# Optimization experiments

Measured on AMD Instinct MI355X. Metric: run time of the kernel, lower is better.

## Reference

```python
import math
import jax, jax.numpy as jnp
import numpy as np

B, S, OBS, ACT, D, H, F, L = 4, 512, 64, 16, 1024, 16, 4096, 4
T = 2 * S - 1  # 1023


def setup_inputs() -> dict:
    key = jax.random.key(0)
    ks = iter(jax.random.split(key, 48))
    def nrm(shape, scale=0.02):
        return (jax.random.normal(next(ks), shape, dtype=jnp.float32) * scale)
    z = lambda *s: jnp.zeros(s, jnp.float32)
    o = lambda *s: jnp.ones(s, jnp.float32)
    inp = {
        'observations': jax.random.normal(next(ks), (B, S, OBS), jnp.float32),
        'actions': jax.random.normal(next(ks), (B, S - 1, ACT), jnp.float32),
        # input_fc: obs_size -> D -> D -> D
        'in_w1': nrm((OBS, D)), 'in_b1': z(D), 'in_w2': nrm((D, D)), 'in_b2': z(D), 'in_w3': nrm((D, D)), 'in_b3': z(D),
        # action_fc: action_size -> D -> D -> D
        'act_w1': nrm((ACT, D)), 'act_b1': z(D), 'act_w2': nrm((D, D)), 'act_b2': z(D), 'act_w3': nrm((D, D)), 'act_b3': z(D),
        # output_fc: D -> D -> D -> action_size
        'out_w1': nrm((D, D)), 'out_b1': z(D), 'out_w2': nrm((D, D)), 'out_b2': z(D), 'out_w3': nrm((D, ACT)), 'out_b3': z(ACT),
        # decoder self-attn (stacked over L layers)
        'sa_w_in': nrm((L, D, 3 * D)), 'sa_b_in': z(L, 3 * D), 'sa_w_out': nrm((L, D, D)), 'sa_b_out': z(L, D),
        # decoder cross-attn
        'ca_w_in': nrm((L, D, 3 * D)), 'ca_b_in': z(L, 3 * D), 'ca_w_out': nrm((L, D, D)), 'ca_b_out': z(L, D),
        # decoder FFN
        'ff_w1': nrm((L, D, F)), 'ff_b1': z(L, F), 'ff_w2': nrm((L, F, D)), 'ff_b2': z(L, D),
        # layer norms
        'ln1_g': o(L, D), 'ln1_b': z(L, D), 'ln2_g': o(L, D), 'ln2_b': z(L, D), 'ln3_g': o(L, D), 'ln3_b': z(L, D),
        'lnf_g': o(D), 'lnf_b': z(D),
    }
    return inp


def _mlp(x, w1, b1, w2, b2, w3, b3):
    x = jax.nn.relu(x @ w1 + b1)
    x = jax.nn.relu(x @ w2 + b2)
    return x @ w3 + b3


def _ln(x, g, b, eps=1e-5):
    mu = x.mean(-1, keepdims=True)
    var = ((x - mu) ** 2).mean(-1, keepdims=True)
    return (x - mu) * jax.lax.rsqrt(var + eps) * g + b


def _mha(q_in, kv_in, w_in, b_in, w_out, b_out, mask):
    Bq, Tq, Dm = q_in.shape
    Tk = kv_in.shape[1]
    dh = Dm // H
    q = q_in @ w_in[:, :Dm] + b_in[:Dm]
    k = kv_in @ w_in[:, Dm:2 * Dm] + b_in[Dm:2 * Dm]
    v = kv_in @ w_in[:, 2 * Dm:] + b_in[2 * Dm:]
    q = q.reshape(Bq, Tq, H, dh).transpose(0, 2, 1, 3)
    k = k.reshape(Bq, Tk, H, dh).transpose(0, 2, 1, 3)
    v = v.reshape(Bq, Tk, H, dh).transpose(0, 2, 1, 3)
    s = jnp.einsum('bhqd,bhkd->bhqk', q, k) / math.sqrt(dh)
    if mask is not None:
        s = s + mask
    a = jax.nn.softmax(s, axis=-1)
    out = jnp.einsum('bhqk,bhkd->bhqd', a, v).transpose(0, 2, 1, 3).reshape(Bq, Tq, Dm)
    return out @ w_out + b_out


def reference(observations, actions,
              in_w1, in_b1, in_w2, in_b2, in_w3, in_b3,
              act_w1, act_b1, act_w2, act_b2, act_w3, act_b3,
              out_w1, out_b1, out_w2, out_b2, out_w3, out_b3,
              sa_w_in, sa_b_in, sa_w_out, sa_b_out,
              ca_w_in, ca_b_in, ca_w_out, ca_b_out,
              ff_w1, ff_b1, ff_w2, ff_b2,
              ln1_g, ln1_b, ln2_g, ln2_b, ln3_g, ln3_b, lnf_g, lnf_b):
    obs_tok = _mlp(observations, in_w1, in_b1, in_w2, in_b2, in_w3, in_b3)   # [B,S,D]
    act_tok = _mlp(actions, act_w1, act_b1, act_w2, act_b2, act_w3, act_b3)  # [B,S-1,D]
    # fused interleave [obs1, act1, obs2, ..., obsS] (replaces the python loops)
    tgt = jnp.zeros((B, T, D), obs_tok.dtype).at[:, 0::2].set(obs_tok).at[:, 1::2].set(act_tok)
    # PositionalEncoding is applied on a batch-first tensor in the original code,
    # so pe[:x.size(0)] indexes by BATCH and broadcasts over the sequence dim (bug-faithful).
    pos = jnp.arange(B, dtype=jnp.float32)[:, None]
    div = jnp.exp(jnp.arange(0, D, 2, dtype=jnp.float32) * (-math.log(10000.0) / D))
    pe = jnp.stack([jnp.sin(pos * div), jnp.cos(pos * div)], axis=-1).reshape(B, D)
    x = tgt + pe[:, None, :]
    mask = jnp.triu(jnp.full((T, T), -jnp.inf, dtype=jnp.float32), k=1)
    mem = jnp.zeros((B, 1, D), x.dtype)  # inp_tok (zero memory token)
    for l in range(L):  # post-norm nn.TransformerDecoderLayer, dropout=0
        x = _ln(x + _mha(x, x, sa_w_in[l], sa_b_in[l], sa_w_out[l], sa_b_out[l], mask), ln1_g[l], ln1_b[l])
        x = _ln(x + _mha(x, mem, ca_w_in[l], ca_b_in[l], ca_w_out[l], ca_b_out[l], None), ln2_g[l], ln2_b[l])
        ff = jax.nn.relu(x @ ff_w1[l] + ff_b1[l]) @ ff_w2[l] + ff_b2[l]
        x = _ln(x + ff, ln3_g[l], ln3_b[l])
    x = _ln(x, lnf_g, lnf_b)  # nn.Transformer final decoder norm
    return _mlp(x, out_w1, out_b1, out_w2, out_b2, out_w3, out_b3)  # [B,T,action_size]
```

## Files before the change

### kernel.cpp

```cpp
#include <hip/hip_runtime.h>
#include <hip/hip_bf16.h>
#include <cstdint>
#include <cstddef>

#define B_  4
#define S_  512
#define T_  1023
#define D_  1024
#define H_  16
#define DH_ 64
#define F_  4096
#define L_  4

typedef float f32x4 __attribute__((ext_vector_type(4)));
typedef __bf16 bf16x8 __attribute__((ext_vector_type(8)));

__device__ inline unsigned pack_bf2(float a, float b) {
    union { __hip_bfloat16 h; unsigned short u; } ua, ub;
    ua.h = __float2bfloat16(a); ub.h = __float2bfloat16(b);
    return (unsigned)ua.u | ((unsigned)ub.u << 16);
}

__global__ __launch_bounds__(256) void gemm_bf16(
    const __hip_bfloat16* __restrict__ A, const __hip_bfloat16* __restrict__ Wt,
    const float* __restrict__ bias,
    float* __restrict__ Cf, __hip_bfloat16* __restrict__ Cb,
    int M, int K, int N, int relu, int ksplit)
{
    __shared__ __align__(16) __hip_bfloat16 AsmB[3][128 * 32];
    __shared__ __align__(16) __hip_bfloat16 BsmB[3][64 * 32];
    const int tid  = threadIdx.x;
    const int lane = tid & 63;
    const int w    = tid >> 6;
    const int wr   = w >> 1, wc = w & 1;
    const int l15  = lane & 15, l4 = lane >> 4;

    const int gx = gridDim.x;
    int bid = blockIdx.y * gx + blockIdx.x;
    {
        const int nwg = gx * gridDim.y;
        const int q = nwg >> 3, r = nwg & 7;
        const int xcd = bid & 7, idx = bid >> 3;
        bid = (xcd < r ? xcd * (q + 1) : r * (q + 1) + (xcd - r) * q) + idx;
    }
    const int row0 = (bid / gx) * 128;
    const int col0 = (bid % gx) * 64;
    const int z = blockIdx.z;
    const int kslice = K / ksplit;
    const int kbase = z * kslice;

    f32x4 acc[4][2] = {};

    auto stage = [&](__hip_bfloat16* As, __hip_bfloat16* Bs, int kt) {
        auto* ldsA = (__attribute__((address_space(3))) char*)As;
        auto* ldsB = (__attribute__((address_space(3))) char*)Bs;
        #pragma unroll
        for (int half = 0; half < 2; ++half) {
            const int ch = half * 256 + tid;
            const int r  = ch >> 2;
            const int c  = (ch & 3) * 8;
            int gr = row0 + r; gr = (gr < M) ? gr : (M - 1);
            const __hip_bfloat16* srcA = A + (size_t)gr * K + kt + c;
            __builtin_amdgcn_global_load_lds(
                (const __attribute__((address_space(1))) unsigned*)srcA,
                (__attribute__((address_space(3))) unsigned*)(ldsA + (size_t)ch * 16),
                16, 0, 0);
        }
        {
            const int r = tid >> 2;
            const int c = (tid & 3) * 8;
            int gc = col0 + r; gc = (gc < N) ? gc : (N - 1);
            const __hip_bfloat16* srcB = Wt + (size_t)gc * K + kt + c;
            __builtin_amdgcn_global_load_lds(
                (const __attribute__((address_space(1))) unsigned*)srcB,
                (__attribute__((address_space(3))) unsigned*)(ldsB + (size_t)tid * 16),
                16, 0, 0);
        }
    };
    auto compute = [&](const __hip_bfloat16* As, const __hip_bfloat16* Bs) {
        const __hip_bfloat16* ab = As + (size_t)(wr * 64 + l15) * 32 + l4 * 8;
        const __hip_bfloat16* bb = Bs + (size_t)(wc * 32 + l15) * 32 + l4 * 8;
        bf16x8 af[4], bf[2];
        #pragma unroll
        for (int mi = 0; mi < 4; ++mi) af[mi] = *(const bf16x8*)(ab + mi * 16 * 32);
        #pragma unroll
        for (int nj = 0; nj < 2; ++nj) bf[nj] = *(const bf16x8*)(bb + nj * 16 * 32);
        #pragma unroll
        for (int mi = 0; mi < 4; ++mi)
            #pragma unroll
            for (int nj = 0; nj < 2; ++nj)
                acc[mi][nj] = __builtin_amdgcn_mfma_f32_16x16x32_bf16(
                    af[mi], bf[nj], acc[mi][nj], 0, 0, 0);
    };

    const int nk = kslice >> 5;
    __hip_bfloat16 *A0 = AsmB[0], *A1 = AsmB[1], *A2 = AsmB[2];
    __hip_bfloat16 *B0 = BsmB[0], *B1 = BsmB[1], *B2 = BsmB[2];
    stage(A0, B0, kbase);
    if (nk > 1) stage(A1, B1, kbase + 32);
    for (int t = 0; t < nk; ++t) {
        if (t + 1 < nk) {
            asm volatile("s_waitcnt vmcnt(3)" ::: "memory");
        } else {
            asm volatile("s_waitcnt vmcnt(0)" ::: "memory");
        }
        __builtin_amdgcn_s_barrier();
        if (t + 2 < nk) stage(A2, B2, kbase + (t + 2) * 32);
        compute(A0, B0);
        __hip_bfloat16* ta = A0; A0 = A1; A1 = A2; A2 = ta;
        __hip_bfloat16* tb = B0; B0 = B1; B1 = B2; B2 = tb;
    }

    if (ksplit > 1) {
        float* dst = Cf + (size_t)z * M * N;
        #pragma unroll
        for (int nj = 0; nj < 2; ++nj) {
            const int c = col0 + wc * 32 + nj * 16 + l15;
            if (c >= N) continue;
            #pragma unroll
            for (int mi = 0; mi < 4; ++mi)
                #pragma unroll
                for (int i = 0; i < 4; ++i) {
                    const int r = row0 + wr * 64 + mi * 16 + l4 * 4 + i;
                    if (r < M) dst[(size_t)r * N + c] = acc[mi][nj][i];
                }
        }
    } else {
        #pragma unroll
        for (int nj = 0; nj < 2; ++nj) {
            const int c = col0 + wc * 32 + nj * 16 + l15;
            if (c >= N) continue;
            const float bv = bias[c];
            #pragma unroll
            for (int mi = 0; mi < 4; ++mi)
                #pragma unroll
                for (int i = 0; i < 4; ++i) {
                    const int r = row0 + wr * 64 + mi * 16 + l4 * 4 + i;
                    if (r >= M) continue;
                    float v = acc[mi][nj][i] + bv;
                    if (relu) v = fmaxf(v, 0.f);
                    if (Cf) Cf[(size_t)r * N + c] = v;
                    if (Cb) Cb[(size_t)r * N + c] = __float2bfloat16(v);
                }
        }
    }
}

__global__ __launch_bounds__(256) void reduce_split(
    const float* __restrict__ part, int SK, size_t pstride,
    const float* __restrict__ bias, int N, int total4, int relu,
    float* __restrict__ outf, __hip_bfloat16* __restrict__ outb)
{
    const int idx4 = blockIdx.x * 256 + threadIdx.x;
    if (idx4 >= total4) return;
    const size_t base = (size_t)idx4 * 4;
    const int c = (int)(base & (size_t)(N - 1));
    float4 v = *(const float4*)(part + base);
    for (int s = 1; s < SK; ++s) {
        const float4 p = *(const float4*)(part + (size_t)s * pstride + base);
        v.x += p.x; v.y += p.y; v.z += p.z; v.w += p.w;
    }
    const float4 bv = *(const float4*)(bias + c);
    v.x += bv.x; v.y += bv.y; v.z += bv.z; v.w += bv.w;
    if (relu) {
        v.x = fmaxf(v.x, 0.f); v.y = fmaxf(v.y, 0.f);
        v.z = fmaxf(v.z, 0.f); v.w = fmaxf(v.w, 0.f);
    }
    if (outf) *(float4*)(outf + base) = v;
    if (outb) {
        __hip_bfloat16* o = outb + base;
        o[0] = __float2bfloat16(v.x); o[1] = __float2bfloat16(v.y);
        o[2] = __float2bfloat16(v.z); o[3] = __float2bfloat16(v.w);
    }
}

__global__ __launch_bounds__(256) void transpose_w(
    const float* __restrict__ W, __hip_bfloat16* __restrict__ Wt,
    int K, int N, int Kpad)
{
    __shared__ float t[32][33];
    W  += (size_t)blockIdx.z * K * N;
    Wt += (size_t)blockIdx.z * N * Kpad;
    const int n0 = blockIdx.x * 32, k0 = blockIdx.y * 32;
    const int tx = threadIdx.x & 31, ty = threadIdx.x >> 5;
    #pragma unroll
    for (int i = 0; i < 4; ++i) {
        int r = ty + i * 8;
        int k = k0 + r, n = n0 + tx;
        t[r][tx] = (k < K && n < N) ? W[(size_t)k * N + n] : 0.f;
    }
    __syncthreads();
    #pragma unroll
    for (int i = 0; i < 4; ++i) {
        int r = ty + i * 8;
        int n = n0 + r, k = k0 + tx;
        if (n < N && k < Kpad) Wt[(size_t)n * Kpad + k] = __float2bfloat16(t[tx][r]);
    }
}

__global__ __launch_bounds__(256) void convert_pad(
    const float* __restrict__ in, __hip_bfloat16* __restrict__ out,
    int M, int Kin, int Kout)
{
    int idx = blockIdx.x * 256 + threadIdx.x;
    if (idx >= M * Kout) return;
    int r = idx / Kout, c = idx - r * Kout;
    out[idx] = __float2bfloat16(c < Kin ? in[(size_t)r * Kin + c] : 0.f);
}

__global__ __launch_bounds__(256) void v_transpose(
    const __hip_bfloat16* __restrict__ qkvb, __hip_bfloat16* __restrict__ vt)
{
    __shared__ __hip_bfloat16 tile[32][33];
    const int b  = blockIdx.z;
    const int c0 = blockIdx.x * 32;
    const int t0 = blockIdx.y * 32;
    const int tx = threadIdx.x & 31, ty = threadIdx.x >> 5;
    const __hip_bfloat16 z = __float2bfloat16(0.f);
    #pragma unroll
    for (int i = 0; i < 4; ++i) {
        const int tl = ty + i * 8;
        const int t = t0 + tl;
        tile[tl][tx] = (t < T_) ? qkvb[(size_t)(b * T_ + t) * 3072 + 2048 + c0 + tx] : z;
    }
    __syncthreads();
    #pragma unroll
    for (int i = 0; i < 4; ++i) {
        const int cl = ty + i * 8;
        const int t = t0 + tx;
        vt[((size_t)(b * 1024 + c0 + cl)) * 1024 + t] = (t < T_) ? tile[tx][cl] : z;
    }
}

__global__ __launch_bounds__(256) void attn_mfma(
    const __hip_bfloat16* __restrict__ qkvb,
    const __hip_bfloat16* __restrict__ vt,
    __hip_bfloat16* __restrict__ out)
{
    __shared__ __align__(16) __hip_bfloat16 Qs[2][128][32];
    __shared__ __align__(16) __hip_bfloat16 Ks[2][64][32];
    __shared__ __align__(16) __hip_bfloat16 Vs[2][64][32];
    __shared__ __align__(16) __hip_bfloat16 Ps[4][2][32][32];
    __shared__ float Lw[4][2][16];

    const int bh = blockIdx.x;
    const int b = bh >> 4, h = bh & 15;
    const int q0 = blockIdx.y * 128;
    const int tid = threadIdx.x;
    const int w = tid >> 6, lane = tid & 63;
    const int l15 = lane & 15, l4 = lane >> 4;
    const size_t ldq = 3 * D_;

    {
        #pragma unroll
        for (int c = 0; c < 2; ++c)
            #pragma unroll
            for (int it = 0; it < 2; ++it) {
                const int ch = it * 256 + tid;
                const int r = ch >> 2, cp = ch & 3;
                int qr = q0 + r; qr = (qr < T_) ? qr : (T_ - 1);
                const __hip_bfloat16* src = qkvb + (size_t)(b * T_ + qr) * ldq + h * 64 + c * 32 + cp * 8;
                __builtin_amdgcn_global_load_lds(
                    (const __attribute__((address_space(1))) unsigned*)src,
                    (__attribute__((address_space(3))) unsigned*)((__attribute__((address_space(3))) char*)&Qs[c][0][0] + ch * 16),
                    16, 0, 0);
            }
    }
    __syncthreads();
    bf16x8 qreg[2][2];
    #pragma unroll
    for (int qf = 0; qf < 2; ++qf)
        #pragma unroll
        for (int c = 0; c < 2; ++c)
            qreg[qf][c] = *(const bf16x8*)&Qs[c][w * 32 + qf * 16 + l15][l4 * 8];

    f32x4 of[2][4] = {};
    float lp[2] = {0.f, 0.f};
    const int qmaxw = q0 + w * 32 + 31;
    const int kend = (q0 + 128 < T_) ? (q0 + 128) : T_;

    for (int k0 = 0; k0 < kend; k0 += 64) {
        __syncthreads();
        {
            const int r = tid >> 2, cp = tid & 3;
            #pragma unroll
            for (int c = 0; c < 2; ++c) {
                int kr = k0 + r; kr = (kr < T_) ? kr : (T_ - 1);
                const __hip_bfloat16* srcK = qkvb + (size_t)(b * T_ + kr) * ldq + D_ + h * 64 + c * 32 + cp * 8;
                __builtin_amdgcn_global_load_lds(
                    (const __attribute__((address_space(1))) unsigned*)srcK,
                    (__attribute__((address_space(3))) unsigned*)((__attribute__((address_space(3))) char*)&Ks[c][0][0] + tid * 16),
                    16, 0, 0);
                const __hip_bfloat16* srcV = vt + ((size_t)(b * 1024 + h * 64 + r)) * 1024 + k0 + c * 32 + cp * 8;
                __builtin_amdgcn_global_load_lds(
                    (const __attribute__((address_space(1))) unsigned*)srcV,
                    (__attribute__((address_space(3))) unsigned*)((__attribute__((address_space(3))) char*)&Vs[c][0][0] + tid * 16),
                    16, 0, 0);
            }
        }
        __syncthreads();

        if (k0 <= qmaxw) {
            f32x4 sf[4][2] = {};
            #pragma unroll
            for (int c = 0; c < 2; ++c) {
                bf16x8 kf[4];
                #pragma unroll
                for (int kfr = 0; kfr < 4; ++kfr)
                    kf[kfr] = *(const bf16x8*)&Ks[c][kfr * 16 + l15][l4 * 8];
                #pragma unroll
                for (int kfr = 0; kfr < 4; ++kfr)
                    #pragma unroll
                    for (int qf = 0; qf < 2; ++qf)
                        sf[kfr][qf] = __builtin_amdgcn_mfma_f32_16x16x32_bf16(
                            kf[kfr], qreg[qf][c], sf[kfr][qf], 0, 0, 0);
            }
            const bool needmask = (k0 + 63) > (q0 + w * 32);
            #pragma unroll
            for (int kfr = 0; kfr < 4; ++kfr) {
                #pragma unroll
                for (int qf = 0; qf < 2; ++qf) {
                    const int qg = q0 + w * 32 + qf * 16 + l15;
                    float p[4];
                    #pragma unroll
                    for (int i = 0; i < 4; ++i) {
                        const int kg = k0 + kfr * 16 + l4 * 4 + i;
                        float pv = __expf(sf[kfr][qf][i] * 0.125f);
                        if (needmask && kg > qg) pv = 0.f;
                        p[i] = pv;
                        lp[qf] += pv;
                    }
                    unsigned* dst = (unsigned*)&Ps[w][kfr >> 1][qf * 16 + l15][(kfr & 1) * 16 + l4 * 4];
                    dst[0] = pack_bf2(p[0], p[1]);
                    dst[1] = pack_bf2(p[2], p[3]);
                }
            }
            #pragma unroll
            for (int kc = 0; kc < 2; ++kc) {
                bf16x8 pa[2], vb[4];
                #pragma unroll
                for (int qf = 0; qf < 2; ++qf)
                    pa[qf] = *(const bf16x8*)&Ps[w][kc][qf * 16 + l15][l4 * 8];
                #pragma unroll
                for (int df = 0; df < 4; ++df)
                    vb[df] = *(const bf16x8*)&Vs[kc][df * 16 + l15][l4 * 8];
                #pragma unroll
                for (int qf = 0; qf < 2; ++qf)
                    #pragma unroll
                    for (int df = 0; df < 4; ++df)
                        of[qf][df] = __builtin_amdgcn_mfma_f32_16x16x32_bf16(
                            pa[qf], vb[df], of[qf][df], 0, 0, 0);
            }
        }
    }

    #pragma unroll
    for (int qf = 0; qf < 2; ++qf) {
        float v = lp[qf];
        v += __shfl_xor(v, 16);
        v += __shfl_xor(v, 32);
        if (l4 == 0) Lw[w][qf][l15] = v;
    }
    __syncthreads();
    #pragma unroll
    for (int qf = 0; qf < 2; ++qf) {
        float inv[4];
        #pragma unroll
        for (int i = 0; i < 4; ++i) inv[i] = 1.f / Lw[w][qf][l4 * 4 + i];
        #pragma unroll
        for (int df = 0; df < 4; ++df) {
            #pragma unroll
            for (int i = 0; i < 4; ++i) {
                const int qg = q0 + w * 32 + qf * 16 + l4 * 4 + i;
                if (qg < T_)
                    out[(size_t)(b * T_ + qg) * D_ + h * 64 + df * 16 + l15] =
                        __float2bfloat16(of[qf][df][i] * inv[i]);
            }
        }
    }
}

__device__ inline void block_ln_stats(float4 v, float& mu, float& inv,
                                      float* ws, float* ws2, float* mu_s, float* inv_s)
{
    const int tid = threadIdx.x;
    float s  = v.x + v.y + v.z + v.w;
    float s2 = v.x * v.x + v.y * v.y + v.z * v.z + v.w * v.w;
    #pragma unroll
    for (int off = 32; off; off >>= 1) {
        s  += __shfl_down(s, off);
        s2 += __shfl_down(s2, off);
    }
    const int wid = tid >> 6;
    if ((tid & 63) == 0) { ws[wid] = s; ws2[wid] = s2; }
    __syncthreads();
    if (tid == 0) {
        float S  = ws[0] + ws[1] + ws[2] + ws[3];
        float S2 = ws2[0] + ws2[1] + ws2[2] + ws2[3];
        float m = S * (1.f / (float)D_);
        float var = S2 * (1.f / (float)D_) - m * m;
        *mu_s = m;
        *inv_s = rsqrtf(var + 1e-5f);
    }
    __syncthreads();
    mu = *mu_s; inv = *inv_s;
}

__global__ __launch_bounds__(256) void add_ln_kernel(
    float* __restrict__ x, const float* __restrict__ p, int SK, size_t pstride,
    const float* __restrict__ pbias,
    const float* __restrict__ g, const float* __restrict__ beta,
    __hip_bfloat16* __restrict__ xb)
{
    const int row = blockIdx.x;
    const int tid = threadIdx.x;
    __shared__ float ws[4], ws2[4], mu_s, inv_s;
    float4* xr = reinterpret_cast<float4*>(x + (size_t)row * D_);
    float4 v = xr[tid];
    if (p) {
        for (int s = 0; s < SK; ++s) {
            const float4 wv = reinterpret_cast<const float4*>(
                p + (size_t)s * pstride + (size_t)row * D_)[tid];
            v.x += wv.x; v.y += wv.y; v.z += wv.z; v.w += wv.w;
        }
        if (pbias) {
            const float4 bv = reinterpret_cast<const float4*>(pbias)[tid];
            v.x += bv.x; v.y += bv.y; v.z += bv.z; v.w += bv.w;
        }
    }
    float mu, inv;
    block_ln_stats(v, mu, inv, ws, ws2, &mu_s, &inv_s);
    const float4 gg = reinterpret_cast<const float4*>(g)[tid];
    const float4 bb = reinterpret_cast<const float4*>(beta)[tid];
    float4 o;
    o.x = (v.x - mu) * inv * gg.x + bb.x;
    o.y = (v.y - mu) * inv * gg.y + bb.y;
    o.z = (v.z - mu) * inv * gg.z + bb.z;
    o.w = (v.w - mu) * inv * gg.w + bb.w;
    xr[tid] = o;
    if (xb) {
        __hip_bfloat16* xo = xb + (size_t)row * D_ + tid * 4;
        xo[0] = __float2bfloat16(o.x);
        xo[1] = __float2bfloat16(o.y);
        xo[2] = __float2bfloat16(o.z);
        xo[3] = __float2bfloat16(o.w);
    }
}

__global__ __launch_bounds__(256) void add_ln2_kernel(
    float* __restrict__ x, const float* __restrict__ p, int SK, size_t pstride,
    const float* __restrict__ pbias, const float* __restrict__ cav,
    const float* __restrict__ g1, const float* __restrict__ b1,
    const float* __restrict__ g2, const float* __restrict__ b2,
    __hip_bfloat16* __restrict__ xb)
{
    const int row = blockIdx.x;
    const int tid = threadIdx.x;
    __shared__ float ws[4], ws2[4], mu_s, inv_s;
    float4* xr = reinterpret_cast<float4*>(x + (size_t)row * D_);
    float4 v = xr[tid];
    for (int s = 0; s < SK; ++s) {
        const float4 wv = reinterpret_cast<const float4*>(
            p + (size_t)s * pstride + (size_t)row * D_)[tid];
        v.x += wv.x; v.y += wv.y; v.z += wv.z; v.w += wv.w;
    }
    if (pbias) {
        const float4 bv = reinterpret_cast<const float4*>(pbias)[tid];
        v.x += bv.x; v.y += bv.y; v.z += bv.z; v.w += bv.w;
    }
    float mu, inv;
    block_ln_stats(v, mu, inv, ws, ws2, &mu_s, &inv_s);
    const float4 g1v = reinterpret_cast<const float4*>(g1)[tid];
    const float4 b1v = reinterpret_cast<const float4*>(b1)[tid];
    const float4 cv  = reinterpret_cast<const float4*>(cav)[tid];
    float4 u;
    u.x = (v.x - mu) * inv * g1v.x + b1v.x + cv.x;
    u.y = (v.y - mu) * inv * g1v.y + b1v.y + cv.y;
    u.z = (v.z - mu) * inv * g1v.z + b1v.z + cv.z;
    u.w = (v.w - mu) * inv * g1v.w + b1v.w + cv.w;
    __syncthreads();
    float mu2, inv2;
    block_ln_stats(u, mu2, inv2, ws, ws2, &mu_s, &inv_s);
    const float4 g2v = reinterpret_cast<const float4*>(g2)[tid];
    const float4 b2v = reinterpret_cast<const float4*>(b2)[tid];
    float4 o;
    o.x = (u.x - mu2) * inv2 * g2v.x + b2v.x;
    o.y = (u.y - mu2) * inv2 * g2v.y + b2v.y;
    o.z = (u.z - mu2) * inv2 * g2v.z + b2v.z;
    o.w = (u.w - mu2) * inv2 * g2v.w + b2v.w;
    xr[tid] = o;
    __hip_bfloat16* xo = xb + (size_t)row * D_ + tid * 4;
    xo[0] = __float2bfloat16(o.x);
    xo[1] = __float2bfloat16(o.y);
    xo[2] = __float2bfloat16(o.z);
    xo[3] = __float2bfloat16(o.w);
}

__global__ __launch_bounds__(256) void interleave_pe_kernel(
    const float* __restrict__ obs_tok, const float* __restrict__ act_tok,
    float* __restrict__ x, __hip_bfloat16* __restrict__ xb)
{
    const int row = blockIdx.x;
    const int b = row / T_;
    const int t = row - b * T_;
    const float* src = (t & 1)
        ? (act_tok + (size_t)(b * (S_ - 1) + (t >> 1)) * D_)
        : (obs_tok + (size_t)(b * S_ + (t >> 1)) * D_);
    float* xr = x + (size_t)row * D_;
    __hip_bfloat16* xo = xb + (size_t)row * D_;
    #pragma unroll
    for (int k = 0; k < 4; ++k) {
        int d = threadIdx.x + k * 256;
        float ang = (float)b * expf(-(float)(d & ~1) * (9.210340371976184f / 1024.0f));
        float pe = (d & 1) ? cosf(ang) : sinf(ang);
        float v = src[d] + pe;
        xr[d] = v;
        xo[d] = __float2bfloat16(v);
    }
}

__global__ __launch_bounds__(256) void ca_part_kernel(
    const float* __restrict__ ca_b_in, const float* __restrict__ ca_w_out,
    float* __restrict__ part)
{
    const int idx = blockIdx.x * 256 + threadIdx.x;
    const int ks = blockIdx.y;
    const int l = idx >> 10, d = idx & 1023;
    const float* bv = ca_b_in + (size_t)l * 3 * D_ + 2 * D_ + ks * 64;
    const float* wp = ca_w_out + (size_t)l * D_ * D_ + (size_t)(ks * 64) * D_ + d;
    float s = 0.f;
    #pragma unroll 8
    for (int k = 0; k < 64; ++k) s = fmaf(bv[k], wp[(size_t)k * D_], s);
    part[(size_t)ks * (L_ * D_) + idx] = s;
}

__global__ __launch_bounds__(256) void ca_reduce_kernel(
    const float* __restrict__ part, const float* __restrict__ ca_b_out,
    float* __restrict__ out)
{
    const int idx = blockIdx.x * 256 + threadIdx.x;
    float s = ca_b_out[idx];
    #pragma unroll
    for (int ks = 0; ks < 16; ++ks) s += part[(size_t)ks * (L_ * D_) + idx];
    out[idx] = s;
}

extern "C" void kernel_launch(void* const* d_in, const int* in_sizes, int n_in,
                              void* d_out, int out_size, void* d_ws, size_t ws_size,
                              hipStream_t stream)
{
    const float* obs     = (const float*)d_in[0];
    const float* act     = (const float*)d_in[1];
    const float* in_w1   = (const float*)d_in[2];
    const float* in_b1   = (const float*)d_in[3];
    const float* in_w2   = (const float*)d_in[4];
    const float* in_b2   = (const float*)d_in[5];
    const float* in_w3   = (const float*)d_in[6];
    const float* in_b3   = (const float*)d_in[7];
    const float* act_w1  = (const float*)d_in[8];
    const float* act_b1  = (const float*)d_in[9];
    const float* act_w2  = (const float*)d_in[10];
    const float* act_b2  = (const float*)d_in[11];
    const float* act_w3  = (const float*)d_in[12];
    const float* act_b3  = (const float*)d_in[13];
    const float* out_w1  = (const float*)d_in[14];
    const float* out_b1  = (const float*)d_in[15];
    const float* out_w2  = (const float*)d_in[16];
    const float* out_b2  = (const float*)d_in[17];
    const float* out_w3  = (const float*)d_in[18];
    const float* out_b3  = (const float*)d_in[19];
    const float* sa_w_in = (const float*)d_in[20];
    const float* sa_b_in = (const float*)d_in[21];
    const float* sa_w_out= (const float*)d_in[22];
    const float* sa_b_out= (const float*)d_in[23];
    const float* ca_b_in = (const float*)d_in[25];
    const float* ca_w_out= (const float*)d_in[26];
    const float* ca_b_out= (const float*)d_in[27];
    const float* ff_w1   = (const float*)d_in[28];
    const float* ff_b1   = (const float*)d_in[29];
    const float* ff_w2   = (const float*)d_in[30];
    const float* ff_b2   = (const float*)d_in[31];
    const float* ln1_g   = (const float*)d_in[32];
    const float* ln1_b   = (const float*)d_in[33];
    const float* ln2_g   = (const float*)d_in[34];
    const float* ln2_b   = (const float*)d_in[35];
    const float* ln3_g   = (const float*)d_in[36];
    const float* ln3_b   = (const float*)d_in[37];
    const float* lnf_g   = (const float*)d_in[38];
    const float* lnf_b   = (const float*)d_in[39];

    const int MT = B_ * T_;
    const int Mo = B_ * S_;
    const int Ma = B_ * (S_ - 1);

    char* base = (char*)d_ws;
    size_t used = 0;
    auto alloc = [&](size_t bytes) -> char* {
        char* r = base + used;
        used += (bytes + 255) & ~(size_t)255;
        return r;
    };
    typedef __hip_bfloat16 bf;
    bf* wi1  = (bf*)alloc((size_t)1024 * 64 * 2);
    bf* wi2  = (bf*)alloc((size_t)1024 * 1024 * 2);
    bf* wi3  = (bf*)alloc((size_t)1024 * 1024 * 2);
    bf* wa1  = (bf*)alloc((size_t)1024 * 32 * 2);
    bf* wa2  = (bf*)alloc((size_t)1024 * 1024 * 2);
    bf* wa3  = (bf*)alloc((size_t)1024 * 1024 * 2);
    bf* wo1  = (bf*)alloc((size_t)1024 * 1024 * 2);
    bf* wo2  = (bf*)alloc((size_t)1024 * 1024 * 2);
    bf* wo3  = (bf*)alloc((size_t)16 * 1024 * 2);
    bf* wsin = (bf*)alloc((size_t)L_ * 3072 * 1024 * 2);
    bf* wsout= (bf*)alloc((size_t)L_ * 1024 * 1024 * 2);
    bf* wf1  = (bf*)alloc((size_t)L_ * 4096 * 1024 * 2);
    bf* wf2  = (bf*)alloc((size_t)L_ * 1024 * 4096 * 2);
    bf* obs_bf = (bf*)alloc((size_t)Mo * 64 * 2);
    bf* act_bf = (bf*)alloc((size_t)Ma * 32 * 2);
    bf* x_bf   = (bf*)alloc((size_t)MT * D_ * 2);
    bf* attnb  = (bf*)alloc((size_t)MT * D_ * 2);
    bf* h1b    = (bf*)alloc((size_t)MT * D_ * 2);
    bf* h2b    = (bf*)alloc((size_t)MT * D_ * 2);
    char* shared_rg = alloc((size_t)MT * F_ * 2);
    bf* qkvb = (bf*)shared_rg;
    bf* ffh  = (bf*)shared_rg;
    bf* vt   = (bf*)alloc((size_t)B_ * 1024 * 1024 * 2);
    float* x       = (float*)alloc((size_t)MT * D_ * 4);
    float* y       = (float*)alloc((size_t)MT * D_ * 4);
    float* obs_tok = (float*)alloc((size_t)Mo * D_ * 4);
    float* act_tok = (float*)alloc((size_t)Ma * D_ * 4);
    float* ca      = (float*)alloc((size_t)L_ * D_ * 4);
    float* ca_part = (float*)alloc((size_t)16 * L_ * D_ * 4);
    if (used > ws_size) return;
    float* part_loop = y;
    float* part_pre  = (float*)shared_rg;
    float* part_post = (float*)shared_rg;

    auto tw = [&](const float* W, bf* Wt, int K, int N, int Kpad, int batch) {
        dim3 g((N + 31) / 32, (Kpad + 31) / 32, batch);
        transpose_w<<<g, 256, 0, stream>>>(W, Wt, K, N, Kpad);
    };
    auto gemm = [&](const bf* A, const bf* Wt, const float* bias,
                    float* Cf, bf* Cb, int M, int K, int N, int relu, int sk) {
        dim3 g((N + 63) / 64, (M + 127) / 128, sk);
        gemm_bf16<<<g, 256, 0, stream>>>(A, Wt, bias, Cf, Cb, M, K, N, relu, sk);
    };
    auto gemm_red = [&](const bf* A, const bf* Wt, const float* bias,
                        float* Cf, bf* Cb, int M, int K, int N, int relu, int sk,
                        float* part) {
        if (sk <= 1) { gemm(A, Wt, bias, Cf, Cb, M, K, N, relu, 1); return; }
        gemm(A, Wt, nullptr, part, nullptr, M, K, N, 0, sk);
        const size_t MN = (size_t)M * N;
        const int total4 = (int)(MN / 4);
        reduce_split<<<(total4 + 255) / 256, 256, 0, stream>>>(
            part, sk, MN, bias, N, total4, relu, Cf, Cb);
    };

    tw(in_w1,  wi1, 64,   1024, 64,   1);
    tw(in_w2,  wi2, 1024, 1024, 1024, 1);
    tw(in_w3,  wi3, 1024, 1024, 1024, 1);
    tw(act_w1, wa1, 16,   1024, 32,   1);
    tw(act_w2, wa2, 1024, 1024, 1024, 1);
    tw(act_w3, wa3, 1024, 1024, 1024, 1);
    tw(out_w1, wo1, 1024, 1024, 1024, 1);
    tw(out_w2, wo2, 1024, 1024, 1024, 1);
    tw(out_w3, wo3, 1024, 16,   1024, 1);
    tw(sa_w_in,  wsin,  1024, 3072, 1024, L_);
    tw(sa_w_out, wsout, 1024, 1024, 1024, L_);
    tw(ff_w1,    wf1,   1024, 4096, 1024, L_);
    tw(ff_w2,    wf2,   4096, 1024, 4096, L_);

    convert_pad<<<(Mo * 64 + 255) / 256, 256, 0, stream>>>(obs, obs_bf, Mo, 64, 64);
    convert_pad<<<(Ma * 32 + 255) / 256, 256, 0, stream>>>(act, act_bf, Ma, 16, 32);
    ca_part_kernel<<<dim3((L_ * D_) / 256, 16), 256, 0, stream>>>(ca_b_in, ca_w_out, ca_part);
    ca_reduce_kernel<<<(L_ * D_) / 256, 256, 0, stream>>>(ca_part, ca_b_out, ca);

    gemm(obs_bf, wi1, in_b1, nullptr, h1b, Mo, 64, D_, 1, 1);
    gemm_red(h1b, wi2, in_b2, nullptr, h2b, Mo, D_, D_, 1, 4, part_pre);
    gemm_red(h2b, wi3, in_b3, obs_tok, nullptr, Mo, D_, D_, 0, 4, part_pre);
    gemm(act_bf, wa1, act_b1, nullptr, h1b, Ma, 32, D_, 1, 1);
    gemm_red(h1b, wa2, act_b2, nullptr, h2b, Ma, D_, D_, 1, 4, part_pre);
    gemm_red(h2b, wa3, act_b3, act_tok, nullptr, Ma, D_, D_, 0, 4, part_pre);

    interleave_pe_kernel<<<MT, 256, 0, stream>>>(obs_tok, act_tok, x, x_bf);

    for (int l = 0; l < L_; ++l) {
        gemm(x_bf, wsin + (size_t)l * 3072 * 1024, sa_b_in + (size_t)l * 3 * D_,
             nullptr, qkvb, MT, D_, 3 * D_, 0, 1);
        v_transpose<<<dim3(32, 32, B_), 256, 0, stream>>>(qkvb, vt);
        attn_mfma<<<dim3(B_ * H_, 8), 256, 0, stream>>>(qkvb, vt, attnb);
        gemm(attnb, wsout + (size_t)l * 1024 * 1024, nullptr,
             part_loop, nullptr, MT, D_, D_, 0, 2);
        add_ln2_kernel<<<MT, 256, 0, stream>>>(x, part_loop, 2, (size_t)MT * D_,
             sa_b_out + (size_t)l * D_, ca + (size_t)l * D_,
             ln1_g + (size_t)l * D_, ln1_b + (size_t)l * D_,
             ln2_g + (size_t)l * D_, ln2_b + (size_t)l * D_, x_bf);
        gemm(x_bf, wf1 + (size_t)l * 4096 * 1024, ff_b1 + (size_t)l * F_,
             nullptr, ffh, MT, D_, F_, 1, 1);
        gemm(ffh, wf2 + (size_t)l * 1024 * 4096, nullptr,
             part_loop, nullptr, MT, F_, D_, 0, 2);
        add_ln_kernel<<<MT, 256, 0, stream>>>(x, part_loop, 2, (size_t)MT * D_,
             ff_b2 + (size_t)l * D_,
             ln3_g + (size_t)l * D_, ln3_b + (size_t)l * D_, x_bf);
    }

    add_ln_kernel<<<MT, 256, 0, stream>>>(x, nullptr, 0, 0, nullptr, lnf_g, lnf_b, x_bf);
    gemm_red(x_bf, wo1, out_b1, nullptr, h1b, MT, D_, D_, 1, 2, part_post);
    gemm_red(h1b,  wo2, out_b2, nullptr, h2b, MT, D_, D_, 1, 2, part_post);
    gemm_red(h2b,  wo3, out_b3, (float*)d_out, nullptr, MT, D_, 16, 0, 8, part_post);
}
```

Baseline: 1.428 ms.

## Batch obs/action MLP GEMMs into paired launches and batch square weight transposes

Merges the observation and action input MLP GEMMs into single paired launches, with the z grid dimension selecting branch and split-K slice, plus a paired reduce kernel. It also folds ten 1024x1024 weight transposes into one launch. The goal is fewer kernel launches and better GPU fill for the small M=2048 GEMMs. Split-K drops from 4 to 2, so each block does more serial K work. The paired buffers assume h1b, h2b and part_pre are large enough to hold both halves.

```diff
diff --git a/kernel.cpp b/kernel.cpp
--- a/kernel.cpp
+++ b/kernel.cpp
@@ -146,6 +146,176 @@
     }
 }
 
+__global__ __launch_bounds__(256) void gemm_pair(
+    const __hip_bfloat16* __restrict__ A0p, const __hip_bfloat16* __restrict__ A1p,
+    const __hip_bfloat16* __restrict__ W0p, const __hip_bfloat16* __restrict__ W1p,
+    const float* __restrict__ b0p, const float* __restrict__ b1p,
+    __hip_bfloat16* __restrict__ Cb0, __hip_bfloat16* __restrict__ Cb1,
+    float* __restrict__ part,
+    int M0, int M1, int K0, int K1, int N, int relu, int sk)
+{
+    __shared__ __align__(16) __hip_bfloat16 AsmB[3][128 * 32];
+    __shared__ __align__(16) __hip_bfloat16 BsmB[3][64 * 32];
+    const int tid  = threadIdx.x;
+    const int lane = tid & 63;
+    const int w    = tid >> 6;
+    const int wr   = w >> 1, wc = w & 1;
+    const int l15  = lane & 15, l4 = lane >> 4;
+
+    const int gx = gridDim.x;
+    int bid = blockIdx.y * gx + blockIdx.x;
+    {
+        const int nwg = gx * gridDim.y;
+        const int q = nwg >> 3, r = nwg & 7;
+        const int xcd = bid & 7, idx = bid >> 3;
+        bid = (xcd < r ? xcd * (q + 1) : r * (q + 1) + (xcd - r) * q) + idx;
+    }
+    const int row0 = (bid / gx) * 128;
+    const int col0 = (bid % gx) * 64;
+
+    const int z = blockIdx.z;
+    const int pair  = z / sk;
+    const int slice = z - pair * sk;
+    const __hip_bfloat16* A  = pair ? A1p : A0p;
+    const __hip_bfloat16* Wt = pair ? W1p : W0p;
+    const float* bias        = pair ? b1p : b0p;
+    const int M = pair ? M1 : M0;
+    const int K = pair ? K1 : K0;
+    const int kslice = K / sk;
+    const int kbase = slice * kslice;
+
+    f32x4 acc[4][2] = {};
+
+    auto stage = [&](__hip_bfloat16* As, __hip_bfloat16* Bs, int kt) {
+        auto* ldsA = (__attribute__((address_space(3))) char*)As;
+        auto* ldsB = (__attribute__((address_space(3))) char*)Bs;
+        #pragma unroll
+        for (int half = 0; half < 2; ++half) {
+            const int ch = half * 256 + tid;
+            const int r  = ch >> 2;
+            const int c  = (ch & 3) * 8;
+            int gr = row0 + r; gr = (gr < M) ? gr : (M - 1);
+            const __hip_bfloat16* srcA = A + (size_t)gr * K + kt + c;
+            __builtin_amdgcn_global_load_lds(
+                (const __attribute__((address_space(1))) unsigned*)srcA,
+                (__attribute__((address_space(3))) unsigned*)(ldsA + (size_t)ch * 16),
+                16, 0, 0);
+        }
+        {
+            const int r = tid >> 2;
+            const int c = (tid & 3) * 8;
+            int gc = col0 + r; gc = (gc < N) ? gc : (N - 1);
+            const __hip_bfloat16* srcB = Wt + (size_t)gc * K + kt + c;
+            __builtin_amdgcn_global_load_lds(
+                (const __attribute__((address_space(1))) unsigned*)srcB,
+                (__attribute__((address_space(3))) unsigned*)(ldsB + (size_t)tid * 16),
+                16, 0, 0);
+        }
+    };
+    auto compute = [&](const __hip_bfloat16* As, const __hip_bfloat16* Bs) {
+        const __hip_bfloat16* ab = As + (size_t)(wr * 64 + l15) * 32 + l4 * 8;
+        const __hip_bfloat16* bb = Bs + (size_t)(wc * 32 + l15) * 32 + l4 * 8;
+        bf16x8 af[4], bf[2];
+        #pragma unroll
+        for (int mi = 0; mi < 4; ++mi) af[mi] = *(const bf16x8*)(ab + mi * 16 * 32);
+        #pragma unroll
+        for (int nj = 0; nj < 2; ++nj) bf[nj] = *(const bf16x8*)(bb + nj * 16 * 32);
+        #pragma unroll
+        for (int mi = 0; mi < 4; ++mi)
+            #pragma unroll
+            for (int nj = 0; nj < 2; ++nj)
+                acc[mi][nj] = __builtin_amdgcn_mfma_f32_16x16x32_bf16(
+                    af[mi], bf[nj], acc[mi][nj], 0, 0, 0);
+    };
+
+    const int nk = kslice >> 5;
+    __hip_bfloat16 *A0 = AsmB[0], *A1 = AsmB[1], *A2 = AsmB[2];
+    __hip_bfloat16 *B0 = BsmB[0], *B1 = BsmB[1], *B2 = BsmB[2];
+    stage(A0, B0, kbase);
+    if (nk > 1) stage(A1, B1, kbase + 32);
+    for (int t = 0; t < nk; ++t) {
+        if (t + 1 < nk) {
+            asm volatile("s_waitcnt vmcnt(3)" ::: "memory");
+        } else {
+            asm volatile("s_waitcnt vmcnt(0)" ::: "memory");
+        }
+        __builtin_amdgcn_s_barrier();
+        if (t + 2 < nk) stage(A2, B2, kbase + (t + 2) * 32);
+        compute(A0, B0);
+        __hip_bfloat16* ta = A0; A0 = A1; A1 = A2; A2 = ta;
+        __hip_bfloat16* tb = B0; B0 = B1; B1 = B2; B2 = tb;
+    }
+
+    if (sk > 1) {
+        const size_t pstride = (size_t)M0 * N;
+        float* dst = part + (size_t)(pair * sk + slice) * pstride;
+        #pragma unroll
+        for (int nj = 0; nj < 2; ++nj) {
+            const int c = col0 + wc * 32 + nj * 16 + l15;
+            #pragma unroll
+            for (int mi = 0; mi < 4; ++mi)
+                #pragma unroll
+                for (int i = 0; i < 4; ++i) {
+                    const int r = row0 + wr * 64 + mi * 16 + l4 * 4 + i;
+                    if (r < M) dst[(size_t)r * N + c] = acc[mi][nj][i];
+                }
+        }
+    } else {
+        __hip_bfloat16* Cb = pair ? Cb1 : Cb0;
+        #pragma unroll
+        for (int nj = 0; nj < 2; ++nj) {
+            const int c = col0 + wc * 32 + nj * 16 + l15;
+            const float bv = bias[c];
+            #pragma unroll
+            for (int mi = 0; mi < 4; ++mi)
+                #pragma unroll
+                for (int i = 0; i < 4; ++i) {
+                    const int r = row0 + wr * 64 + mi * 16 + l4 * 4 + i;
+                    if (r >= M) continue;
+                    float v = acc[mi][nj][i] + bv;
+                    if (relu) v = fmaxf(v, 0.f);
+                    Cb[(size_t)r * N + c] = __float2bfloat16(v);
+                }
+        }
+    }
+}
+
+__global__ __launch_bounds__(256) void reduce_pair(
+    const float* __restrict__ part, size_t pstride, int sk,
+    const float* __restrict__ b0p, const float* __restrict__ b1p,
+    int M0, int M1, int N, int relu,
+    __hip_bfloat16* __restrict__ ob0, __hip_bfloat16* __restrict__ ob1,
+    float* __restrict__ of0, float* __restrict__ of1)
+{
+    const int pair = blockIdx.y;
+    const int Mp = pair ? M1 : M0;
+    const int idx4 = blockIdx.x * 256 + threadIdx.x;
+    if (idx4 >= (Mp * N) / 4) return;
+    const size_t base = (size_t)idx4 * 4;
+    const int c = (int)(base & (size_t)(N - 1));
+    const float* p0 = part + (size_t)(pair * sk) * pstride;
+    float4 v = *(const float4*)(p0 + base);
+    for (int s = 1; s < sk; ++s) {
+        const float4 p = *(const float4*)(p0 + (size_t)s * pstride + base);
+        v.x += p.x; v.y += p.y; v.z += p.z; v.w += p.w;
+    }
+    const float* bias = pair ? b1p : b0p;
+    const float4 bv = *(const float4*)(bias + c);
+    v.x += bv.x; v.y += bv.y; v.z += bv.z; v.w += bv.w;
+    if (relu) {
+        v.x = fmaxf(v.x, 0.f); v.y = fmaxf(v.y, 0.f);
+        v.z = fmaxf(v.z, 0.f); v.w = fmaxf(v.w, 0.f);
+    }
+    __hip_bfloat16* ob = pair ? ob1 : ob0;
+    float* of = pair ? of1 : of0;
+    if (of) *(float4*)(of + base) = v;
+    if (ob) {
+        __hip_bfloat16* o = ob + base;
+        o[0] = __float2bfloat16(v.x); o[1] = __float2bfloat16(v.y);
+        o[2] = __float2bfloat16(v.z); o[3] = __float2bfloat16(v.w);
+    }
+}
+
 __global__ __launch_bounds__(256) void reduce_split(
     const float* __restrict__ part, int SK, size_t pstride,
     const float* __restrict__ bias, int N, int total4, int relu,
@@ -195,6 +365,28 @@
         int r = ty + i * 8;
         int n = n0 + r, k = k0 + tx;
         if (n < N && k < Kpad) Wt[(size_t)n * Kpad + k] = __float2bfloat16(t[tx][r]);
+    }
+}
+
+struct TW10 { const float* src[10]; __hip_bfloat16* dst[10]; };
+
+__global__ __launch_bounds__(256) void transpose_w_b(TW10 p)
+{
+    __shared__ float t[32][33];
+    const float* W = p.src[blockIdx.z];
+    __hip_bfloat16* Wt = p.dst[blockIdx.z];
+    const int n0 = blockIdx.x * 32, k0 = blockIdx.y * 32;
+    const int tx = threadIdx.x & 31, ty = threadIdx.x >> 5;
+    #pragma unroll
+    for (int i = 0; i < 4; ++i) {
+        int r = ty + i * 8;
+        t[r][tx] = W[(size_t)(k0 + r) * 1024 + n0 + tx];
+    }
+    __syncthreads();
+    #pragma unroll
+    for (int i = 0; i < 4; ++i) {
+        int r = ty + i * 8;
+        Wt[(size_t)(n0 + r) * 1024 + k0 + tx] = __float2bfloat16(t[tx][r]);
     }
 }
 
@@ -655,31 +847,48 @@
             part, sk, MN, bias, N, total4, relu, Cf, Cb);
     };
 
+    {
+        TW10 p;
+        p.src[0] = in_w2;  p.dst[0] = wi2;
+        p.src[1] = in_w3;  p.dst[1] = wi3;
+        p.src[2] = act_w2; p.dst[2] = wa2;
+        p.src[3] = act_w3; p.dst[3] = wa3;
+        p.src[4] = out_w1; p.dst[4] = wo1;
+        p.src[5] = out_w2; p.dst[5] = wo2;
+        for (int l = 0; l < L_; ++l) {
+            p.src[6 + l] = sa_w_out + (size_t)l * 1024 * 1024;
+            p.dst[6 + l] = wsout + (size_t)l * 1024 * 1024;
+        }
+        transpose_w_b<<<dim3(32, 32, 10), 256, 0, stream>>>(p);
+    }
     tw(in_w1,  wi1, 64,   1024, 64,   1);
-    tw(in_w2,  wi2, 1024, 1024, 1024, 1);
-    tw(in_w3,  wi3, 1024, 1024, 1024, 1);
     tw(act_w1, wa1, 16,   1024, 32,   1);
-    tw(act_w2, wa2, 1024, 1024, 1024, 1);
-    tw(act_w3, wa3, 1024, 1024, 1024, 1);
-    tw(out_w1, wo1, 1024, 1024, 1024, 1);
-    tw(out_w2, wo2, 1024, 1024, 1024, 1);
     tw(out_w3, wo3, 1024, 16,   1024, 1);
-    tw(sa_w_in,  wsin,  1024, 3072, 1024, L_);
-    tw(sa_w_out, wsout, 1024, 1024, 1024, L_);
-    tw(ff_w1,    wf1,   1024, 4096, 1024, L_);
-    tw(ff_w2,    wf2,   4096, 1024, 4096, L_);
+    tw(sa_w_in, wsin, 1024, 3072, 1024, L_);
+    tw(ff_w1,   wf1,  1024, 4096, 1024, L_);
+    tw(ff_w2,   wf2,  4096, 1024, 4096, L_);
 
     convert_pad<<<(Mo * 64 + 255) / 256, 256, 0, stream>>>(obs, obs_bf, Mo, 64, 64);
     convert_pad<<<(Ma * 32 + 255) / 256, 256, 0, stream>>>(act, act_bf, Ma, 16, 32);
     ca_part_kernel<<<dim3((L_ * D_) / 256, 16), 256, 0, stream>>>(ca_b_in, ca_w_out, ca_part);
     ca_reduce_kernel<<<(L_ * D_) / 256, 256, 0, stream>>>(ca_part, ca_b_out, ca);
 
-    gemm(obs_bf, wi1, in_b1, nullptr, h1b, Mo, 64, D_, 1, 1);
-    gemm_red(h1b, wi2, in_b2, nullptr, h2b, Mo, D_, D_, 1, 4, part_pre);
-    gemm_red(h2b, wi3, in_b3, obs_tok, nullptr, Mo, D_, D_, 0, 4, part_pre);
-    gemm(act_bf, wa1, act_b1, nullptr, h1b, Ma, 32, D_, 1, 1);
-    gemm_red(h1b, wa2, act_b2, nullptr, h2b, Ma, D_, D_, 1, 4, part_pre);
-    gemm_red(h2b, wa3, act_b3, act_tok, nullptr, Ma, D_, D_, 0, 4, part_pre);
+    const size_t MoD = (size_t)Mo * D_;
+    gemm_pair<<<dim3(16, 16, 2), 256, 0, stream>>>(
+        obs_bf, act_bf, wi1, wa1, in_b1, act_b1,
+        h1b, h1b + MoD, nullptr, Mo, Ma, 64, 32, D_, 1, 1);
+    gemm_pair<<<dim3(16, 16, 4), 256, 0, stream>>>(
+        h1b, h1b + MoD, wi2, wa2, nullptr, nullptr,
+        nullptr, nullptr, part_pre, Mo, Ma, D_, D_, D_, 0, 2);
+    reduce_pair<<<dim3((int)(MoD / 4 + 255) / 256, 2), 256, 0, stream>>>(
+        part_pre, MoD, 2, in_b2, act_b2, Mo, Ma, D_, 1,
+        h2b, h2b + MoD, nullptr, nullptr);
+    gemm_pair<<<dim3(16, 16, 4), 256, 0, stream>>>(
+        h2b, h2b + MoD, wi3, wa3, nullptr, nullptr,
+        nullptr, nullptr, part_pre, Mo, Ma, D_, D_, D_, 0, 2);
+    reduce_pair<<<dim3((int)(MoD / 4 + 255) / 256, 2), 256, 0, stream>>>(
+        part_pre, MoD, 2, in_b3, act_b3, Mo, Ma, D_, 0,
+        nullptr, nullptr, obs_tok, act_tok);
 
     interleave_pe_kernel<<<MT, 256, 0, stream>>>(obs_tok, act_tok, x, x_bf);
 
```

Result: faster. 1.362 ms (-4.7%).
